# Optimization experiments

Measured on AMD Instinct MI355X. Metric: run time of the kernel, lower is better.

## Reference

```python
import jax, jax.numpy as jnp
import numpy as np

DIM = 128
HEADS = 4
DIM_HEAD = 32
EPS = 1e-5


def layer_norm(x, w, b):
    mu = jnp.mean(x, axis=-1, keepdims=True)
    var = jnp.mean(jnp.square(x - mu), axis=-1, keepdims=True)
    return (x - mu) * jax.lax.rsqrt(var + EPS) * w + b


def setup_inputs() -> dict:
    key = jax.random.key(0)
    ks = jax.random.split(key, 16)
    B, N, D, bH, bW = 2, 6, DIM, 50, 50
    iH, iW = 24, 56
    HD = HEADS * DIM_HEAD
    w = lambda k, shp: (jax.random.normal(k, shp, jnp.float32) * 0.02)
    inp = {
        "q": jax.random.normal(ks[0], (B, N, D, bH, bW), jnp.float32),
        "k": jax.random.normal(ks[1], (B, N, D, iH, iW), jnp.float32),
        "v": jax.random.normal(ks[2], (B, N, D, iH, iW), jnp.float32),
        "skip": jax.random.normal(ks[3], (B, D, bH, bW), jnp.float32),
        "ln_q_w": jnp.ones((D,), jnp.float32), "ln_q_b": jnp.zeros((D,), jnp.float32),
        "wq": w(ks[4], (D, HD)), "bq": jnp.zeros((HD,), jnp.float32),
        "ln_k_w": jnp.ones((D,), jnp.float32), "ln_k_b": jnp.zeros((D,), jnp.float32),
        "wk": w(ks[5], (D, HD)), "bk": jnp.zeros((HD,), jnp.float32),
        "ln_v_w": jnp.ones((D,), jnp.float32), "ln_v_b": jnp.zeros((D,), jnp.float32),
        "wv": w(ks[6], (D, HD)), "bv": jnp.zeros((HD,), jnp.float32),
        "wo": w(ks[7], (HD, D)), "bo": jnp.zeros((D,), jnp.float32),
        "ln_pre_w": jnp.ones((D,), jnp.float32), "ln_pre_b": jnp.zeros((D,), jnp.float32),
        "w1": w(ks[8], (D, 2 * D)), "b1": jnp.zeros((2 * D,), jnp.float32),
        "w2": w(ks[9], (2 * D, D)), "b2": jnp.zeros((D,), jnp.float32),
        "ln_post_w": jnp.ones((D,), jnp.float32), "ln_post_b": jnp.zeros((D,), jnp.float32),
    }
    return inp


def reference(q, k, v, skip,
              ln_q_w, ln_q_b, wq, bq,
              ln_k_w, ln_k_b, wk, bk,
              ln_v_w, ln_v_b, wv, bv,
              wo, bo, ln_pre_w, ln_pre_b,
              w1, b1, w2, b2, ln_post_w, ln_post_b):
    B, N, D, bH, bW = q.shape
    iH, iW = k.shape[-2:]
    Q, K = bH * bW, iH * iW
    scale = D ** (-0.5)  # NOTE: original uses dim**-0.5, not dim_head

    # queries: (B,N,D,Q) -> (B,N,Q,D) -> LN -> linear -> (B,N,Q,H,Dh)
    qf = jnp.transpose(q.reshape(B, N, D, Q), (0, 1, 3, 2))
    qh = (layer_norm(qf, ln_q_w, ln_q_b) @ wq + bq).reshape(B, N, Q, HEADS, DIM_HEAD)
    # keys: (B,N,D,K) -> (B,N,K,D)
    kf = jnp.transpose(k.reshape(B, N, D, K), (0, 1, 3, 2))
    kh = (layer_norm(kf, ln_k_w, ln_k_b) @ wk + bk).reshape(B, N, K, HEADS, DIM_HEAD)
    # values: (B,N,D,iH,iW) -> (B,N,iH,iW,D) -> (B,N*K,D)
    vf = jnp.transpose(v, (0, 1, 3, 4, 2)).reshape(B, N * K, D)
    vh = (layer_norm(vf, ln_v_w, ln_v_b) @ wv + bv).reshape(B, N * K, HEADS, DIM_HEAD)

    # logits: (B,N,Q,K,H) -> (B,Q,N*K,H), softmax over combined N*K axis
    logits = scale * jnp.einsum('bnqmd,bnkmd->bnqkm', qh, kh)
    logits = jnp.transpose(logits, (0, 2, 1, 3, 4)).reshape(B, Q, N * K, HEADS)
    att = jax.nn.softmax(logits, axis=-2)

    a = jnp.einsum('bqkm,bkmd->bqmd', att, vh).reshape(B, Q, HEADS * DIM_HEAD)
    z = a @ wo + bo  # (B,Q,D)
    z = z + jnp.transpose(skip.reshape(B, D, Q), (0, 2, 1))
    z = layer_norm(z, ln_pre_w, ln_pre_b)
    z = z + (jax.nn.gelu(z @ w1 + b1, approximate=False) @ w2 + b2)
    z = layer_norm(z, ln_post_w, ln_post_b)
    return jnp.transpose(z.reshape(B, bH, bW, D), (0, 3, 1, 2))
```

## Files before the change

kernel.cpp:

```cpp
#include <hip/hip_runtime.h>
#include <hip/hip_bf16.h>

#define QP 2500
#define KP 1344
#define SCALE 0.088388347648318447f
#define LOG2E 1.4426950408889634f
#define LNEPS 1e-5f

typedef __attribute__((ext_vector_type(8))) short bf16x8;
typedef __attribute__((ext_vector_type(4))) float f32x4;

__device__ inline ushort f2bf(float x) {
  uint u = __float_as_uint(x);
  return (ushort)((u + 0x7fffu + ((u >> 16) & 1u)) >> 16);
}

union Frag8 { uint2 u[2]; bf16x8 f; ushort us[8]; };

__device__ inline bf16x8 ldfrag_swz(const char* rowbase, int colbyte, int C) {
  Frag8 t;
  t.u[0] = *(const uint2*)(rowbase + ((colbyte) ^ C));
  t.u[1] = *(const uint2*)(rowbase + ((colbyte + 8) ^ C));
  return t.f;
}

__device__ inline uint pk2(float a, float b) {
  union { __hip_bfloat162 h; uint u; } cv;
  cv.h = __float22bfloat162_rn(make_float2(a, b));
  return cv.u;
}

__device__ inline void gld16(const ushort* g, ushort* l) {
  __builtin_amdgcn_global_load_lds(
      (const __attribute__((address_space(1))) void*)g,
      (__attribute__((address_space(3))) void*)l, 16, 0, 0);
}

__global__ __launch_bounds__(256) void wprep_kernel(
    const float* __restrict__ wq, const float* __restrict__ wk, const float* __restrict__ wv,
    ushort* __restrict__ wtq, ushort* __restrict__ wtk, ushort* __restrict__ wtv)
{
  const float* W = (blockIdx.y == 0) ? wq : (blockIdx.y == 1) ? wk : wv;
  ushort* WT = (blockIdx.y == 0) ? wtq : (blockIdx.y == 1) ? wtk : wtv;
  const int t = threadIdx.x;
  const int idx = blockIdx.x * 1024 + t * 4;
  const int k = idx >> 7, j0 = idx & 127;
  float4 rd = *(const float4*)&W[idx];
  WT[(j0 + 0) * 128 + k] = f2bf(rd.x);
  WT[(j0 + 1) * 128 + k] = f2bf(rd.y);
  WT[(j0 + 2) * 128 + k] = f2bf(rd.z);
  WT[(j0 + 3) * 128 + k] = f2bf(rd.w);
}

__global__ __launch_bounds__(256) void wprep2_kernel(
    const float* __restrict__ wo, const float* __restrict__ w1, const float* __restrict__ w2,
    ushort* __restrict__ woT, ushort* __restrict__ w1T, ushort* __restrict__ w2T)
{
  const int y = blockIdx.y;
  const float* W; ushort* WT; int jsh, K, total;
  if (y == 0)      { W = wo; WT = woT; jsh = 7; K = 128; total = 16384; }
  else if (y == 1) { W = w1; WT = w1T; jsh = 8; K = 128; total = 32768; }
  else             { W = w2; WT = w2T; jsh = 7; K = 256; total = 32768; }
  const int idx = blockIdx.x * 1024 + threadIdx.x * 4;
  if (idx >= total) return;
  const int k = idx >> jsh, j0 = idx & ((1 << jsh) - 1);
  float4 rd = *(const float4*)&W[idx];
  WT[(j0 + 0) * K + k] = f2bf(rd.x);
  WT[(j0 + 1) * K + k] = f2bf(rd.y);
  WT[(j0 + 2) * K + k] = f2bf(rd.z);
  WT[(j0 + 3) * K + k] = f2bf(rd.w);
}

__global__ __launch_bounds__(256) void proj_kernel(
    const float* __restrict__ qin, const float* __restrict__ kin, const float* __restrict__ vin,
    const float* __restrict__ lnqw, const float* __restrict__ lnqb,
    const float* __restrict__ lnkw, const float* __restrict__ lnkb,
    const float* __restrict__ lnvw, const float* __restrict__ lnvb,
    const ushort* __restrict__ wtq_, const ushort* __restrict__ wtk_, const ushort* __restrict__ wtv_,
    const float* __restrict__ bq_, const float* __restrict__ bk_, const float* __restrict__ bv_,
    ushort* __restrict__ qout, ushort* __restrict__ kout, ushort* __restrict__ vtout)
{
  const int z = blockIdx.z;
  if (z > 0 && blockIdx.x >= 21) return;

  const float *in, *lnw, *lnb, *bias;
  const ushort* WT;
  int P;
  if (z == 0)      { in = qin; lnw = lnqw; lnb = lnqb; WT = wtq_; bias = bq_; P = QP; }
  else if (z == 1) { in = kin; lnw = lnkw; lnb = lnkb; WT = wtk_; bias = bk_; P = KP; }
  else             { in = vin; lnw = lnvw; lnb = lnvb; WT = wtv_; bias = bv_; P = KP; }

  __shared__ __align__(16) ushort xb[64][128];
  __shared__ __align__(16) ushort wt[128][128];
  __shared__ float ps[4][64], pq[4][64];
  __shared__ float mu_s[64], rs_s[64];

  const int bn = blockIdx.y;
  const int p0 = blockIdx.x * 64;
  const int t  = threadIdx.x;
  const int w = t >> 6, lane = t & 63, g = lane >> 4, ln15 = lane & 15;

  #pragma unroll
  for (int i = 0; i < 8; ++i) {
    int idx8 = t + 256 * i;
    int j = idx8 >> 4, ck = (idx8 & 15) * 16;
    *(uint4*)((char*)wt + j * 256 + (ck ^ ((j & 7) << 4))) =
        *(const uint4*)((const char*)WT + j * 256 + ck);
  }

  const float* src = in + ((size_t)bn * 128) * P + p0;
  const int p = t & 63, dq = t >> 6;
  float xv[32];
  float s = 0.f, s2 = 0.f;
  #pragma unroll
  for (int kk = 0; kk < 32; ++kk) {
    int d = dq + 4 * kk;
    float v = (p0 + p < P) ? src[(size_t)d * P + p] : 0.f;
    xv[kk] = v; s += v; s2 += v * v;
  }
  ps[dq][p] = s; pq[dq][p] = s2;
  __syncthreads();
  if (t < 64) {
    float a = ps[0][t] + ps[1][t] + ps[2][t] + ps[3][t];
    float b = pq[0][t] + pq[1][t] + pq[2][t] + pq[3][t];
    float mu = a * (1.f / 128.f);
    float var = b * (1.f / 128.f) - mu * mu;
    mu_s[t] = mu; rs_s[t] = rsqrtf(var + LNEPS);
  }
  __syncthreads();
  {
    const float mu = mu_s[p], rs = rs_s[p];
    const int CW = (p & 7) << 4;
    #pragma unroll
    for (int kk = 0; kk < 32; ++kk) {
      int d = dq + 4 * kk;
      float v = (xv[kk] - mu) * rs * lnw[d] + lnb[d];
      *(ushort*)((char*)xb + p * 256 + ((2 * d) ^ CW)) = f2bf(v);
    }
  }
  __syncthreads();

  const int prow = w * 16 + ln15;
  const char* xrow = (const char*)xb + prow * 256;
  const int CX = (prow & 7) << 4;
  const int CB = (ln15 & 7) << 4;
  const f32x4 zf = {0.f, 0.f, 0.f, 0.f};
  f32x4 acc[8];
  #pragma unroll
  for (int jc = 0; jc < 8; ++jc) acc[jc] = zf;

  #pragma unroll
  for (int ks = 0; ks < 4; ++ks) {
    bf16x8 a = ldfrag_swz(xrow, ks * 64 + g * 16, CX);
    #pragma unroll
    for (int jc = 0; jc < 8; ++jc) {
      bf16x8 b = ldfrag_swz((const char*)wt + (jc * 16 + ln15) * 256, ks * 64 + g * 16, CB);
      acc[jc] = __builtin_amdgcn_mfma_f32_16x16x32_bf16(a, b, acc[jc], 0, 0, 0);
    }
  }

  if (z == 0) {
    const float os = SCALE * LOG2E;
    #pragma unroll
    for (int jc = 0; jc < 8; ++jc) {
      const float bj = bias[jc * 16 + ln15];
      #pragma unroll
      for (int r = 0; r < 4; ++r) {
        int pr = p0 + w * 16 + 4 * g + r;
        if (pr < P)
          qout[((size_t)bn * P + pr) * 128 + jc * 16 + ln15] = f2bf((acc[jc][r] + bj) * os);
      }
    }
  } else if (z == 1) {
    #pragma unroll
    for (int jc = 0; jc < 8; ++jc) {
      const int j = jc * 16 + ln15;
      const int h = j >> 5, dh = j & 31, gk = dh >> 3, pos = dh & 7;
      const float bj = bias[j];
      #pragma unroll
      for (int r4 = 0; r4 < 4; ++r4) {
        int pp = p0 + w * 16 + 4 * g + r4;
        int kt = pp >> 6, r = pp & 63;
        int ch = (gk + (r >> 1)) & 3;
        kout[(size_t)((bn * 4 + h) * 21 + kt) * 2048 + r * 32 + ch * 8 + pos] =
            f2bf(acc[jc][r4] + bj);
      }
    }
  } else {
    #pragma unroll
    for (int jc = 0; jc < 8; ++jc) {
      const int j = jc * 16 + ln15;
      const int h = j >> 5, rdh = j & 31;
      const float bj = bias[j];
      #pragma unroll
      for (int r4 = 0; r4 < 4; ++r4) {
        int pp = p0 + w * 16 + 4 * g + r4;
        int kt = pp >> 6, kk = pp & 63;
        int ch = (kk >> 3) ^ (rdh & 7);
        vtout[(size_t)((bn * 4 + h) * 21 + kt) * 2048 + rdh * 64 + ch * 8 + (kk & 7)] =
            f2bf(acc[jc][r4] + bj);
      }
    }
  }
}

__global__ __launch_bounds__(256, 4) void attn_kernel(
    const ushort* __restrict__ qh, const ushort* __restrict__ kimg,
    const ushort* __restrict__ vimg, float* __restrict__ aw,
    float* __restrict__ ml)
{
  __shared__ __align__(16) ushort Kb[2][2048];
  __shared__ __align__(16) ushort Vb[2][2048];
  __shared__ __align__(16) ushort Ps[4][16][64];

  const int lin = blockIdx.x + 40 * (blockIdx.y + 4 * blockIdx.z);
  const int sid = (lin & 7) * 240 + (lin >> 3);
  const int bx = sid % 40;
  const int hh = (sid / 40) & 3;
  const int bn = sid / 160;

  const int q0 = bx * 64;
  const int t = threadIdx.x;
  const int w = t >> 6, lane = t & 63;
  const int g = lane >> 4, ln15 = lane & 15;
  const int C = ((ln15 & 7) << 4) | (((ln15 >> 3) & 1) << 3);
  const int kch = (g + (ln15 >> 1)) & 3;
  const int vch0 = (0 + g) ^ (ln15 & 7);
  const int vch1 = (4 + g) ^ (ln15 & 7);

  bf16x8 qf;
  {
    Frag8 z_; z_.u[0] = make_uint2(0, 0); z_.u[1] = make_uint2(0, 0);
    int qr = q0 + w * 16 + ln15;
    qf = (qr < QP) ? *(const bf16x8*)&qh[((size_t)bn * QP + qr) * 128 + hh * 32 + g * 8] : z_.f;
  }

  Frag8 onesU;
  #pragma unroll
  for (int i = 0; i < 8; ++i) onesU.us[i] = 0x3F80;
  const bf16x8 ones = onesU.f;

  const ushort* ksrc = kimg + (size_t)((bn * 4 + hh) * 21) * 2048 + w * 512 + lane * 8;
  const ushort* vsrc = vimg + (size_t)((bn * 4 + hh) * 21) * 2048 + w * 512 + lane * 8;

  gld16(ksrc, &Kb[0][w * 512]);
  gld16(vsrc, &Vb[0][w * 512]);
  __syncthreads();

  const f32x4 zf = {0.f, 0.f, 0.f, 0.f};
  f32x4 o0 = zf, o1 = zf, ol = zf;

  for (int kt = 0; kt < 21; ++kt) {
    const int cur = kt & 1;
    if (kt < 20) {
      gld16(ksrc + (size_t)(kt + 1) * 2048, &Kb[cur ^ 1][w * 512]);
      gld16(vsrc + (size_t)(kt + 1) * 2048, &Vb[cur ^ 1][w * 512]);
    }

    const char* Kbase = (const char*)Kb[cur];
    const char* Vbase = (const char*)Vb[cur];
    char* Pw = (char*)Ps[w];

    f32x4 s[4];
    #pragma unroll
    for (int kb = 0; kb < 4; ++kb) {
      bf16x8 kf = *(const bf16x8*)(Kbase + (kb * 16 + ln15) * 64 + kch * 16);
      s[kb] = __builtin_amdgcn_mfma_f32_16x16x32_bf16(kf, qf, zf, 0, 0, 0);
    }

    {
      char* pr = Pw + ln15 * 128;
      #pragma unroll
      for (int kb = 0; kb < 4; ++kb) {
        uint2 u;
        u.x = pk2(exp2f(s[kb][0]), exp2f(s[kb][1]));
        u.y = pk2(exp2f(s[kb][2]), exp2f(s[kb][3]));
        *(uint2*)(pr + ((kb * 32 + g * 8) ^ C)) = u;
      }
    }

    {
      const char* pr = Pw + ln15 * 128;
      #pragma unroll
      for (int kc = 0; kc < 2; ++kc) {
        bf16x8 pa = ldfrag_swz(pr, kc * 64 + g * 16, C);
        const int vch = kc ? vch1 : vch0;
        bf16x8 vf0 = *(const bf16x8*)(Vbase + ln15 * 128 + vch * 16);
        bf16x8 vf1 = *(const bf16x8*)(Vbase + (16 + ln15) * 128 + vch * 16);
        o0 = __builtin_amdgcn_mfma_f32_16x16x32_bf16(pa, vf0, o0, 0, 0, 0);
        o1 = __builtin_amdgcn_mfma_f32_16x16x32_bf16(pa, vf1, o1, 0, 0, 0);
        ol = __builtin_amdgcn_mfma_f32_16x16x32_bf16(pa, ones, ol, 0, 0, 0);
      }
    }
    __syncthreads();
  }

  if (ln15 == 0) {
    #pragma unroll
    for (int i = 0; i < 4; ++i) {
      int qr = q0 + w * 16 + 4 * g + i;
      if (qr < QP) ml[((size_t)bn * QP + qr) * 4 + hh] = ol[i];
    }
  }
  #pragma unroll
  for (int i = 0; i < 4; ++i) {
    int qr = q0 + w * 16 + 4 * g + i;
    if (qr < QP) {
      size_t base = ((size_t)bn * QP + qr) * 128 + hh * 32;
      aw[base + ln15] = o0[i];
      aw[base + 16 + ln15] = o1[i];
    }
  }
}

__global__ __launch_bounds__(256) void epilogue_kernel(
    const float* __restrict__ aw, const float* __restrict__ ml,
    const float* __restrict__ skip,
    const ushort* __restrict__ woT, const float* __restrict__ bo,
    const float* __restrict__ lnpw, const float* __restrict__ lnpb,
    const ushort* __restrict__ w1T, const float* __restrict__ b1,
    const ushort* __restrict__ w2T, const float* __restrict__ b2,
    const float* __restrict__ lnqw, const float* __restrict__ lnqb,
    float* __restrict__ out)
{
  __shared__ __align__(16) ushort xa[16][128];
  __shared__ __align__(16) ushort znb[16][128];
  __shared__ __align__(16) ushort hb[16][256];
  __shared__ float skp[128][17];
  __shared__ float2 red[4][16];
  __shared__ float mu_s[16], rs_s[16];
  __shared__ float cc[16][4];

  const int b = blockIdx.y;
  const int q0 = blockIdx.x * 16;
  const int t = threadIdx.x;
  const int w = t >> 6, lane = t & 63, g = lane >> 4, ln15 = lane & 15;
  const f32x4 zf = {0.f, 0.f, 0.f, 0.f};

  if (t < 64) {
    int r = t >> 2, h = t & 3;
    int qrow = q0 + r;
    float inv = 0.f;
    if (qrow < QP) {
      float sum = 0.f;
      #pragma unroll
      for (int n = 0; n < 6; ++n)
        sum += ml[((size_t)(b * 6 + n) * QP + qrow) * 4 + h];
      inv = 1.f / sum;
    }
    cc[r][h] = inv;
  }
  #pragma unroll
  for (int i = 0; i < 8; ++i) {
    int idx = t + 256 * i;
    int j = idx >> 4, r = idx & 15;
    int qrow = q0 + r;
    skp[j][r] = (qrow < QP) ? skip[((size_t)b * 128 + j) * QP + qrow] : 0.f;
  }
  __syncthreads();

  #pragma unroll
  for (int i = 0; i < 4; ++i) {
    int idx = t + 256 * i;
    int r = idx >> 6, jp = idx & 63;
    int qrow = q0 + r;
    float v0 = 0.f, v1 = 0.f;
    if (qrow < QP) {
      #pragma unroll
      for (int n = 0; n < 6; ++n) {
        float2 p = *(const float2*)&aw[((size_t)(b * 6 + n) * QP + qrow) * 128 + 2 * jp];
        v0 += p.x; v1 += p.y;
      }
      float iv = cc[r][jp >> 4];
      v0 *= iv; v1 *= iv;
    }
    *(uint*)((char*)xa + r * 256 + ((4 * jp) ^ ((r & 7) << 4))) = pk2(v0, v1);
  }
  __syncthreads();

  f32x4 acc1[2] = {zf, zf};
  #pragma unroll
  for (int ks = 0; ks < 4; ++ks) {
    bf16x8 a = ldfrag_swz((const char*)xa + ln15 * 256, ks * 64 + g * 16, (ln15 & 7) << 4);
    #pragma unroll
    for (int jc = 0; jc < 2; ++jc) {
      int j = (2 * w + jc) * 16 + ln15;
      bf16x8 bfr = *(const bf16x8*)&woT[j * 128 + ks * 32 + g * 8];
      acc1[jc] = __builtin_amdgcn_mfma_f32_16x16x32_bf16(a, bfr, acc1[jc], 0, 0, 0);
    }
  }
  float z[2][4];
  #pragma unroll
  for (int jc = 0; jc < 2; ++jc) {
    int j = (2 * w + jc) * 16 + ln15;
    float bj = bo[j];
    #pragma unroll
    for (int i = 0; i < 4; ++i)
      z[jc][i] = acc1[jc][i] + bj + skp[j][4 * g + i];
  }
  {
    float s_[4], q_[4];
    #pragma unroll
    for (int i = 0; i < 4; ++i) {
      s_[i] = z[0][i] + z[1][i];
      q_[i] = z[0][i] * z[0][i] + z[1][i] * z[1][i];
    }
    #pragma unroll
    for (int m = 1; m <= 8; m <<= 1) {
      #pragma unroll
      for (int i = 0; i < 4; ++i) {
        s_[i] += __shfl_xor(s_[i], m);
        q_[i] += __shfl_xor(q_[i], m);
      }
    }
    if (ln15 == 0) {
      #pragma unroll
      for (int i = 0; i < 4; ++i) red[w][4 * g + i] = make_float2(s_[i], q_[i]);
    }
  }
  __syncthreads();
  if (t < 16) {
    float S = red[0][t].x + red[1][t].x + red[2][t].x + red[3][t].x;
    float Q = red[0][t].y + red[1][t].y + red[2][t].y + red[3][t].y;
    float mu = S * (1.f / 128.f);
    float var = Q * (1.f / 128.f) - mu * mu;
    mu_s[t] = mu; rs_s[t] = rsqrtf(var + LNEPS);
  }
  __syncthreads();
  float zn[2][4];
  #pragma unroll
  for (int jc = 0; jc < 2; ++jc) {
    int j = (2 * w + jc) * 16 + ln15;
    float lw = lnpw[j], lb = lnpb[j];
    #pragma unroll
    for (int i = 0; i < 4; ++i) {
      int r = 4 * g + i;
      float v = (z[jc][i] - mu_s[r]) * rs_s[r] * lw + lb;
      zn[jc][i] = v;
      *(ushort*)((char*)znb + r * 256 + ((2 * j) ^ ((r & 7) << 4))) = f2bf(v);
    }
  }
  __syncthreads();

  f32x4 acc2[4] = {zf, zf, zf, zf};
  #pragma unroll
  for (int ks = 0; ks < 4; ++ks) {
    bf16x8 a = ldfrag_swz((const char*)znb + ln15 * 256, ks * 64 + g * 16, (ln15 & 7) << 4);
    #pragma unroll
    for (int jc2 = 0; jc2 < 4; ++jc2) {
      int j2 = (4 * w + jc2) * 16 + ln15;
      bf16x8 bfr = *(const bf16x8*)&w1T[j2 * 128 + ks * 32 + g * 8];
      acc2[jc2] = __builtin_amdgcn_mfma_f32_16x16x32_bf16(a, bfr, acc2[jc2], 0, 0, 0);
    }
  }
  #pragma unroll
  for (int jc2 = 0; jc2 < 4; ++jc2) {
    int j2 = (4 * w + jc2) * 16 + ln15;
    float bj = b1[j2];
    #pragma unroll
    for (int i = 0; i < 4; ++i) {
      float x = acc2[jc2][i] + bj;
      float ge = 0.5f * x * (1.f + erff(x * 0.70710678118654752f));
      int r = 4 * g + i;
      *(ushort*)((char*)hb + r * 512 + ((2 * j2) ^ ((r & 7) << 4))) = f2bf(ge);
    }
  }
  __syncthreads();

  f32x4 acc3[2] = {zf, zf};
  #pragma unroll
  for (int ks = 0; ks < 8; ++ks) {
    bf16x8 a = ldfrag_swz((const char*)hb + ln15 * 512, ks * 64 + g * 16, (ln15 & 7) << 4);
    #pragma unroll
    for (int jc = 0; jc < 2; ++jc) {
      int j = (2 * w + jc) * 16 + ln15;
      bf16x8 bfr = *(const bf16x8*)&w2T[j * 256 + ks * 32 + g * 8];
      acc3[jc] = __builtin_amdgcn_mfma_f32_16x16x32_bf16(a, bfr, acc3[jc], 0, 0, 0);
    }
  }
  float z2[2][4];
  #pragma unroll
  for (int jc = 0; jc < 2; ++jc) {
    int j = (2 * w + jc) * 16 + ln15;
    float bj = b2[j];
    #pragma unroll
    for (int i = 0; i < 4; ++i)
      z2[jc][i] = acc3[jc][i] + bj + zn[jc][i];
  }
  {
    float s_[4], q_[4];
    #pragma unroll
    for (int i = 0; i < 4; ++i) {
      s_[i] = z2[0][i] + z2[1][i];
      q_[i] = z2[0][i] * z2[0][i] + z2[1][i] * z2[1][i];
    }
    #pragma unroll
    for (int m = 1; m <= 8; m <<= 1) {
      #pragma unroll
      for (int i = 0; i < 4; ++i) {
        s_[i] += __shfl_xor(s_[i], m);
        q_[i] += __shfl_xor(q_[i], m);
      }
    }
    if (ln15 == 0) {
      #pragma unroll
      for (int i = 0; i < 4; ++i) red[w][4 * g + i] = make_float2(s_[i], q_[i]);
    }
  }
  __syncthreads();
  if (t < 16) {
    float S = red[0][t].x + red[1][t].x + red[2][t].x + red[3][t].x;
    float Q = red[0][t].y + red[1][t].y + red[2][t].y + red[3][t].y;
    float mu = S * (1.f / 128.f);
    float var = Q * (1.f / 128.f) - mu * mu;
    mu_s[t] = mu; rs_s[t] = rsqrtf(var + LNEPS);
  }
  __syncthreads();
  #pragma unroll
  for (int jc = 0; jc < 2; ++jc) {
    int j = (2 * w + jc) * 16 + ln15;
    float lw = lnqw[j], lb = lnqb[j];
    #pragma unroll
    for (int i = 0; i < 4; ++i) {
      int r = 4 * g + i;
      skp[j][r] = (z2[jc][i] - mu_s[r]) * rs_s[r] * lw + lb;
    }
  }
  __syncthreads();
  #pragma unroll
  for (int i = 0; i < 8; ++i) {
    int idx = t + 256 * i;
    int j = idx >> 4, r = idx & 15;
    int qrow = q0 + r;
    if (qrow < QP)
      out[((size_t)b * 128 + j) * QP + qrow] = skp[j][r];
  }
}

extern "C" void kernel_launch(void* const* d_in, const int* in_sizes, int n_in,
                              void* d_out, int out_size, void* d_ws, size_t ws_size,
                              hipStream_t stream) {
  const float* q       = (const float*)d_in[0];
  const float* k       = (const float*)d_in[1];
  const float* v       = (const float*)d_in[2];
  const float* skip    = (const float*)d_in[3];
  const float* ln_q_w  = (const float*)d_in[4];
  const float* ln_q_b  = (const float*)d_in[5];
  const float* wq      = (const float*)d_in[6];
  const float* bq      = (const float*)d_in[7];
  const float* ln_k_w  = (const float*)d_in[8];
  const float* ln_k_b  = (const float*)d_in[9];
  const float* wk      = (const float*)d_in[10];
  const float* bk      = (const float*)d_in[11];
  const float* ln_v_w  = (const float*)d_in[12];
  const float* ln_v_b  = (const float*)d_in[13];
  const float* wv      = (const float*)d_in[14];
  const float* bv      = (const float*)d_in[15];
  const float* wo      = (const float*)d_in[16];
  const float* bo      = (const float*)d_in[17];
  const float* ln_pre_w  = (const float*)d_in[18];
  const float* ln_pre_b  = (const float*)d_in[19];
  const float* w1      = (const float*)d_in[20];
  const float* b1      = (const float*)d_in[21];
  const float* w2      = (const float*)d_in[22];
  const float* b2      = (const float*)d_in[23];
  const float* ln_post_w = (const float*)d_in[24];
  const float* ln_post_b = (const float*)d_in[25];

  float* out = (float*)d_out;
  ushort* qhp  = (ushort*)d_ws;
  ushort* kimg = qhp + 3840000;
  ushort* vimg = kimg + 2064384;
  ushort* wtq  = vimg + 2064384;
  ushort* wtk  = wtq + 16384;
  ushort* wtv  = wtk + 16384;
  ushort* woT  = wtv + 16384;
  ushort* w1T  = woT + 16384;
  ushort* w2T  = w1T + 32768;
  float*  aw   = (float*)(w2T + 32768);
  float*  ml   = aw + 3840000;

  wprep_kernel<<<dim3(16, 3), 256, 0, stream>>>(wq, wk, wv, wtq, wtk, wtv);
  wprep2_kernel<<<dim3(32, 3), 256, 0, stream>>>(wo, w1, w2, woT, w1T, w2T);
  proj_kernel<<<dim3(40, 12, 3), 256, 0, stream>>>(q, k, v,
      ln_q_w, ln_q_b, ln_k_w, ln_k_b, ln_v_w, ln_v_b,
      wtq, wtk, wtv, bq, bk, bv, qhp, kimg, vimg);
  attn_kernel<<<dim3(40, 4, 12), 256, 0, stream>>>(qhp, kimg, vimg, aw, ml);
  epilogue_kernel<<<dim3(157, 2), 256, 0, stream>>>(aw, ml, skip, woT, bo,
      ln_pre_w, ln_pre_b, w1T, b1, w2T, b2, ln_post_w, ln_post_b, out);
}
```

Measured before the change: 110.2 us.

## Switch attention to 32x32x16 MFMA with in-register P via permlane32 swap

The attention kernel now uses 128-thread blocks in which each wave owns 32 query rows and computes S and P·V with 32x32x16 bf16 MFMAs. Shared-memory staging of the P tile is removed: the exponentiated scores are packed and redistributed across lane halves with v_permlane32_swap. The row-sum is accumulated in registers instead of through an extra MFMA against a ones vector. The K image layout written by the projection kernel is re-swizzled to match the new fragment loads. This targets LDS round-trips and wasted MFMA work, at the cost of more registers per thread and fewer waves per block.

```diff
diff --git a/kernel.cpp b/kernel.cpp
--- a/kernel.cpp
+++ b/kernel.cpp
@@ -9,6 +9,7 @@
 
 typedef __attribute__((ext_vector_type(8))) short bf16x8;
 typedef __attribute__((ext_vector_type(4))) float f32x4;
+typedef __attribute__((ext_vector_type(16))) float f32x16;
 
 __device__ inline ushort f2bf(float x) {
   uint u = __float_as_uint(x);
@@ -175,14 +176,16 @@
     #pragma unroll
     for (int jc = 0; jc < 8; ++jc) {
       const int j = jc * 16 + ln15;
-      const int h = j >> 5, dh = j & 31, gk = dh >> 3, pos = dh & 7;
+      const int h = j >> 5, dh32 = j & 31;
+      const int c = dh32 >> 3, e = dh32 & 7;
       const float bj = bias[j];
       #pragma unroll
       for (int r4 = 0; r4 < 4; ++r4) {
         int pp = p0 + w * 16 + 4 * g + r4;
         int kt = pp >> 6, r = pp & 63;
-        int ch = (gk + (r >> 1)) & 3;
-        kout[(size_t)((bn * 4 + h) * 21 + kt) * 2048 + r * 32 + ch * 8 + pos] =
+        int l2 = r >> 1;
+        int pz = ((r & 1) * 4 + c + l2) & 7;
+        kout[(size_t)((bn * 4 + h) * 21 + kt) * 2048 + l2 * 64 + pz * 8 + e] =
             f2bf(acc[jc][r4] + bj);
       }
     }
@@ -204,14 +207,13 @@
   }
 }
 
-__global__ __launch_bounds__(256, 4) void attn_kernel(
+__global__ __launch_bounds__(128, 4) void attn_kernel(
     const ushort* __restrict__ qh, const ushort* __restrict__ kimg,
     const ushort* __restrict__ vimg, float* __restrict__ aw,
     float* __restrict__ ml)
 {
   __shared__ __align__(16) ushort Kb[2][2048];
   __shared__ __align__(16) ushort Vb[2][2048];
-  __shared__ __align__(16) ushort Ps[4][16][64];
 
   const int lin = blockIdx.x + 40 * (blockIdx.y + 4 * blockIdx.z);
   const int sid = (lin & 7) * 240 + (lin >> 3);
@@ -221,95 +223,100 @@
 
   const int q0 = bx * 64;
   const int t = threadIdx.x;
-  const int w = t >> 6, lane = t & 63;
-  const int g = lane >> 4, ln15 = lane & 15;
-  const int C = ((ln15 & 7) << 4) | (((ln15 >> 3) & 1) << 3);
-  const int kch = (g + (ln15 >> 1)) & 3;
-  const int vch0 = (0 + g) ^ (ln15 & 7);
-  const int vch1 = (4 + g) ^ (ln15 & 7);
-
-  bf16x8 qf;
+  const int w = t >> 6;
+  const int lane = t & 63;
+  const int lk = lane & 31;
+  const int hi = lane >> 5;
+
+  bf16x8 qf0, qf1;
   {
     Frag8 z_; z_.u[0] = make_uint2(0, 0); z_.u[1] = make_uint2(0, 0);
-    int qr = q0 + w * 16 + ln15;
-    qf = (qr < QP) ? *(const bf16x8*)&qh[((size_t)bn * QP + qr) * 128 + hh * 32 + g * 8] : z_.f;
-  }
-
-  Frag8 onesU;
-  #pragma unroll
-  for (int i = 0; i < 8; ++i) onesU.us[i] = 0x3F80;
-  const bf16x8 ones = onesU.f;
-
-  const ushort* ksrc = kimg + (size_t)((bn * 4 + hh) * 21) * 2048 + w * 512 + lane * 8;
-  const ushort* vsrc = vimg + (size_t)((bn * 4 + hh) * 21) * 2048 + w * 512 + lane * 8;
-
-  gld16(ksrc, &Kb[0][w * 512]);
-  gld16(vsrc, &Vb[0][w * 512]);
-  __syncthreads();
-
-  const f32x4 zf = {0.f, 0.f, 0.f, 0.f};
-  f32x4 o0 = zf, o1 = zf, ol = zf;
+    int qrow = q0 + w * 32 + lk;
+    if (qrow < QP) {
+      const ushort* qp = &qh[((size_t)bn * QP + qrow) * 128 + hh * 32 + hi * 8];
+      qf0 = *(const bf16x8*)(qp);
+      qf1 = *(const bf16x8*)(qp + 16);
+    } else { qf0 = z_.f; qf1 = z_.f; }
+  }
+
+  const ushort* ksrc = kimg + (size_t)((bn * 4 + hh) * 21) * 2048 + w * 1024 + lane * 8;
+  const ushort* vsrc = vimg + (size_t)((bn * 4 + hh) * 21) * 2048 + w * 1024 + lane * 8;
+
+  gld16(ksrc,       &Kb[0][w * 1024]);
+  gld16(ksrc + 512, &Kb[0][w * 1024 + 512]);
+  gld16(vsrc,       &Vb[0][w * 1024]);
+  gld16(vsrc + 512, &Vb[0][w * 1024 + 512]);
+  __syncthreads();
+
+  f32x16 O;
+  #pragma unroll
+  for (int i = 0; i < 16; ++i) O[i] = 0.f;
+  float lpart = 0.f;
 
   for (int kt = 0; kt < 21; ++kt) {
     const int cur = kt & 1;
     if (kt < 20) {
-      gld16(ksrc + (size_t)(kt + 1) * 2048, &Kb[cur ^ 1][w * 512]);
-      gld16(vsrc + (size_t)(kt + 1) * 2048, &Vb[cur ^ 1][w * 512]);
-    }
-
+      const ushort* kp = ksrc + (size_t)(kt + 1) * 2048;
+      const ushort* vp = vsrc + (size_t)(kt + 1) * 2048;
+      gld16(kp,       &Kb[cur ^ 1][w * 1024]);
+      gld16(kp + 512, &Kb[cur ^ 1][w * 1024 + 512]);
+      gld16(vp,       &Vb[cur ^ 1][w * 1024]);
+      gld16(vp + 512, &Vb[cur ^ 1][w * 1024 + 512]);
+    }
     const char* Kbase = (const char*)Kb[cur];
     const char* Vbase = (const char*)Vb[cur];
-    char* Pw = (char*)Ps[w];
-
-    f32x4 s[4];
-    #pragma unroll
-    for (int kb = 0; kb < 4; ++kb) {
-      bf16x8 kf = *(const bf16x8*)(Kbase + (kb * 16 + ln15) * 64 + kch * 16);
-      s[kb] = __builtin_amdgcn_mfma_f32_16x16x32_bf16(kf, qf, zf, 0, 0, 0);
-    }
-
-    {
-      char* pr = Pw + ln15 * 128;
-      #pragma unroll
-      for (int kb = 0; kb < 4; ++kb) {
-        uint2 u;
-        u.x = pk2(exp2f(s[kb][0]), exp2f(s[kb][1]));
-        u.y = pk2(exp2f(s[kb][2]), exp2f(s[kb][3]));
-        *(uint2*)(pr + ((kb * 32 + g * 8) ^ C)) = u;
-      }
-    }
-
-    {
-      const char* pr = Pw + ln15 * 128;
-      #pragma unroll
-      for (int kc = 0; kc < 2; ++kc) {
-        bf16x8 pa = ldfrag_swz(pr, kc * 64 + g * 16, C);
-        const int vch = kc ? vch1 : vch0;
-        bf16x8 vf0 = *(const bf16x8*)(Vbase + ln15 * 128 + vch * 16);
-        bf16x8 vf1 = *(const bf16x8*)(Vbase + (16 + ln15) * 128 + vch * 16);
-        o0 = __builtin_amdgcn_mfma_f32_16x16x32_bf16(pa, vf0, o0, 0, 0, 0);
-        o1 = __builtin_amdgcn_mfma_f32_16x16x32_bf16(pa, vf1, o1, 0, 0, 0);
-        ol = __builtin_amdgcn_mfma_f32_16x16x32_bf16(pa, ones, ol, 0, 0, 0);
-      }
+
+    #pragma unroll
+    for (int kc2 = 0; kc2 < 2; ++kc2) {
+      f32x16 S;
+      #pragma unroll
+      for (int i = 0; i < 16; ++i) S[i] = 0.f;
+      {
+        const int l2 = kc2 * 16 + (lk >> 1);
+        const int pb = (lk & 1) * 4 + hi + l2;
+        bf16x8 kfa = *(const bf16x8*)(Kbase + l2 * 128 + ((pb + 0) & 7) * 16);
+        bf16x8 kfb = *(const bf16x8*)(Kbase + l2 * 128 + ((pb + 2) & 7) * 16);
+        S = __builtin_amdgcn_mfma_f32_32x32x16_bf16(kfa, qf0, S, 0, 0, 0);
+        S = __builtin_amdgcn_mfma_f32_32x32x16_bf16(kfb, qf1, S, 0, 0, 0);
+      }
+
+      float e0 = exp2f(S[0]),  e1 = exp2f(S[1]),  e2 = exp2f(S[2]),  e3 = exp2f(S[3]);
+      float e4 = exp2f(S[4]),  e5 = exp2f(S[5]),  e6 = exp2f(S[6]),  e7 = exp2f(S[7]);
+      float e8 = exp2f(S[8]),  e9 = exp2f(S[9]),  e10 = exp2f(S[10]), e11 = exp2f(S[11]);
+      float e12 = exp2f(S[12]), e13 = exp2f(S[13]), e14 = exp2f(S[14]), e15 = exp2f(S[15]);
+      lpart += (((e0 + e1) + (e2 + e3)) + ((e4 + e5) + (e6 + e7)))
+             + (((e8 + e9) + (e10 + e11)) + ((e12 + e13) + (e14 + e15)));
+      uint w0 = pk2(e0, e1),  w1 = pk2(e2, e3),  w2 = pk2(e4, e5),  w3 = pk2(e6, e7);
+      uint w4 = pk2(e8, e9),  w5 = pk2(e10, e11), w6 = pk2(e12, e13), w7 = pk2(e14, e15);
+
+      asm volatile("v_permlane32_swap_b32 %0, %1" : "+v"(w2), "+v"(w0));
+      asm volatile("v_permlane32_swap_b32 %0, %1" : "+v"(w3), "+v"(w1));
+      asm volatile("v_permlane32_swap_b32 %0, %1" : "+v"(w6), "+v"(w4));
+      asm volatile("v_permlane32_swap_b32 %0, %1" : "+v"(w7), "+v"(w5));
+
+      Frag8 pa0, pa1;
+      pa0.u[0] = make_uint2(w0, w1); pa0.u[1] = make_uint2(w2, w3);
+      pa1.u[0] = make_uint2(w4, w5); pa1.u[1] = make_uint2(w6, w7);
+      bf16x8 vf0 = *(const bf16x8*)(Vbase + lk * 128 + (((kc2 * 4 + 0 + hi) ^ (lk & 7)) * 16));
+      bf16x8 vf1 = *(const bf16x8*)(Vbase + lk * 128 + (((kc2 * 4 + 2 + hi) ^ (lk & 7)) * 16));
+      O = __builtin_amdgcn_mfma_f32_32x32x16_bf16(pa0.f, vf0, O, 0, 0, 0);
+      O = __builtin_amdgcn_mfma_f32_32x32x16_bf16(pa1.f, vf1, O, 0, 0, 0);
     }
     __syncthreads();
   }
 
-  if (ln15 == 0) {
-    #pragma unroll
-    for (int i = 0; i < 4; ++i) {
-      int qr = q0 + w * 16 + 4 * g + i;
-      if (qr < QP) ml[((size_t)bn * QP + qr) * 4 + hh] = ol[i];
-    }
-  }
-  #pragma unroll
-  for (int i = 0; i < 4; ++i) {
-    int qr = q0 + w * 16 + 4 * g + i;
-    if (qr < QP) {
-      size_t base = ((size_t)bn * QP + qr) * 128 + hh * 32;
-      aw[base + ln15] = o0[i];
-      aw[base + 16 + ln15] = o1[i];
-    }
+  float lsum = lpart + __shfl_xor(lpart, 32);
+  {
+    int qrow = q0 + w * 32 + lk;
+    if (hi == 0 && qrow < QP)
+      ml[((size_t)bn * QP + qrow) * 4 + hh] = lsum;
+  }
+  #pragma unroll
+  for (int reg = 0; reg < 16; ++reg) {
+    int crow = (reg & 3) + 8 * (reg >> 2) + 4 * hi;
+    int qrow = q0 + w * 32 + crow;
+    if (qrow < QP)
+      aw[((size_t)bn * QP + qrow) * 128 + hh * 32 + lk] = O[reg];
   }
 }
 
@@ -585,7 +592,7 @@
   proj_kernel<<<dim3(40, 12, 3), 256, 0, stream>>>(q, k, v,
       ln_q_w, ln_q_b, ln_k_w, ln_k_b, ln_v_w, ln_v_b,
       wtq, wtk, wtv, bq, bk, bv, qhp, kimg, vimg);
-  attn_kernel<<<dim3(40, 4, 12), 256, 0, stream>>>(qhp, kimg, vimg, aw, ml);
+  attn_kernel<<<dim3(40, 4, 12), 128, 0, stream>>>(qhp, kimg, vimg, aw, ml);
   epilogue_kernel<<<dim3(157, 2), 256, 0, stream>>>(aw, ml, skip, woT, bo,
       ln_pre_w, ln_pre_b, w1T, b1, w2T, b2, ln_post_w, ln_post_b, out);
 }
```

Result: slower. 126.5 us (+14.8%).
